# Kernel optimization log

Measured on AMD Instinct MI355X. Metric: run time of the kernel, lower is better.

## Reference

```python
import jax, jax.numpy as jnp
import numpy as np

VOCAB, D = 100000, 300
B, L = 256, 1000
H, C = 512, 5


def setup_inputs() -> dict:
    key = jax.random.key(0)
    ks = jax.random.split(key, 9)
    emb = jax.random.normal(ks[0], (VOCAB, D), dtype=jnp.float32) * 0.1
    W1 = jax.random.normal(ks[1], (D, H), dtype=jnp.float32) * (1.0 / np.sqrt(D))
    b1 = jnp.zeros((H,), dtype=jnp.float32)
    W2 = jax.random.normal(ks[2], (H, H), dtype=jnp.float32) * (1.0 / np.sqrt(H))
    b2 = jnp.zeros((H,), dtype=jnp.float32)
    W3 = jax.random.normal(ks[3], (H, C), dtype=jnp.float32) * (1.0 / np.sqrt(H))
    b3 = jnp.zeros((C,), dtype=jnp.float32)
    docs = jax.random.randint(ks[4], (B, L), 0, VOCAB, dtype=jnp.int32)
    doc_lens = jax.random.randint(ks[5], (B,), 1, L + 1, dtype=jnp.int32)
    return {"embeddings": emb, "W1": W1, "b1": b1, "W2": W2, "b2": b2,
            "W3": W3, "b3": b3, "docs": docs, "doc_lens": doc_lens}


def reference(embeddings, W1, b1, W2, b2, W3, b3, docs, doc_lens):
    # Fused gather + segment-mean: [B, L, D] -> [B, D]
    gathered = embeddings[docs]                       # [B, L, D]
    avg = gathered.sum(axis=1) / doc_lens.astype(jnp.float32)[:, None]  # [B, D]
    # MLP: in -> hidden (ReLU) -> hidden (ReLU) -> classes
    h = jax.nn.relu(avg @ W1 + b1)
    h = jax.nn.relu(h @ W2 + b2)
    return h @ W3 + b3                                # [B, C]
```

## Files before the change

### kernel.cpp

```cpp
#include <hip/hip_runtime.h>

#define VOCAB 100000
#define D     300
#define B     256
#define L     1000
#define H     512
#define C     5

#define D4f    (D / 4)
#define NPH    8
#define RW     1563
#define SELCAP 384

#define WS_PARTIAL 0
#define WS_AVG     (B * 8 * D)
#define WS_H1      (WS_AVG + B * D)
#define WS_H2      (WS_H1 + B * H)

__global__ __launch_bounds__(320) void gather_phased_kernel(
    const float* __restrict__ emb, const int* __restrict__ docs,
    float* __restrict__ partial) {
  const int bid = blockIdx.x;
  const int x = bid & 7;
  const int j = bid >> 3;
  const int t = threadIdx.x;
  const int g = t / 80;
  const int lane = t - g * 80;

  __shared__ int    s_raw[2][L];
  __shared__ int    s_sel[2][SELCAP];
  __shared__ int    s_cnt[2][NPH];
  __shared__ int    s_off[2][NPH + 1];
  __shared__ float4 sred[4][2][D4f];

  for (int i = t; i < 2 * L; i += 320) {
    const int dd = i < L ? 0 : 1;
    const int ii = dd ? i - L : i;
    s_raw[dd][ii] = docs[(size_t)(j * 2 + dd) * L + ii];
  }
  if (t < 2 * NPH) s_cnt[t >> 3][t & 7] = 0;
  __syncthreads();

  for (int i = t; i < 2 * L; i += 320) {
    const int dd = i < L ? 0 : 1;
    const int idx = s_raw[dd][dd ? i - L : i];
    const int r = idx / RW;
    if ((r & 7) == x) atomicAdd(&s_cnt[dd][r >> 3], 1);
  }
  __syncthreads();
  if (t < 2) {
    int acc = 0;
#pragma unroll
    for (int p = 0; p < NPH; ++p) { s_off[t][p] = acc; acc += s_cnt[t][p]; }
    s_off[t][NPH] = acc;
  }
  __syncthreads();
  if (t < 2 * NPH) s_cnt[t >> 3][t & 7] = 0;
  __syncthreads();

  for (int i = t; i < 2 * L; i += 320) {
    const int dd = i < L ? 0 : 1;
    const int idx = s_raw[dd][dd ? i - L : i];
    const int r = idx / RW;
    if ((r & 7) == x) {
      const int pos = s_off[dd][r >> 3] + atomicAdd(&s_cnt[dd][r >> 3], 1);
      s_sel[dd][pos] = idx;
    }
  }
  __syncthreads();

  float4 a0 = make_float4(0.f, 0.f, 0.f, 0.f);
  float4 a1 = make_float4(0.f, 0.f, 0.f, 0.f);
  if (lane < D4f) {
    for (int p = 0; p < NPH; ++p) {
      {
        const int s = s_off[0][p], e = s_off[0][p + 1];
        for (int i = s + g; i < e; i += 4) {
          const float4 v = reinterpret_cast<const float4*>(
              emb + (size_t)s_sel[0][i] * D)[lane];
          a0.x += v.x; a0.y += v.y; a0.z += v.z; a0.w += v.w;
        }
      }
      {
        const int s = s_off[1][p], e = s_off[1][p + 1];
        for (int i = s + g; i < e; i += 4) {
          const float4 v = reinterpret_cast<const float4*>(
              emb + (size_t)s_sel[1][i] * D)[lane];
          a1.x += v.x; a1.y += v.y; a1.z += v.z; a1.w += v.w;
        }
      }
    }
    sred[g][0][lane] = a0;
    sred[g][1][lane] = a1;
  }
  __syncthreads();

  if (t < 2 * D4f) {
    const int dd = t / D4f, c4 = t - dd * D4f;
    float ax = 0.f, ay = 0.f, az = 0.f, aw = 0.f;
#pragma unroll
    for (int gg = 0; gg < 4; ++gg) {
      const float4 v = sred[gg][dd][c4];
      ax += v.x; ay += v.y; az += v.z; aw += v.w;
    }
    reinterpret_cast<float4*>(partial +
                              (size_t)((j * 2 + dd) * 8 + x) * D)[c4] =
        make_float4(ax, ay, az, aw);
  }
}

__global__ __launch_bounds__(128) void avg_kernel(
    const float* __restrict__ partial, const int* __restrict__ dlen,
    float* __restrict__ avg) {
  const int b = blockIdx.x;
  const int t = threadIdx.x;
  if (t < D4f) {
    const float4* p =
        reinterpret_cast<const float4*>(partial) + (size_t)b * 8 * D4f + t;
    float4 v[8];
#pragma unroll
    for (int xx = 0; xx < 8; ++xx) v[xx] = p[xx * D4f];
    float ax = 0.f, ay = 0.f, az = 0.f, aw = 0.f;
#pragma unroll
    for (int xx = 0; xx < 8; ++xx) {
      ax += v[xx].x; ay += v[xx].y; az += v[xx].z; aw += v[xx].w;
    }
    const float inv = 1.f / (float)dlen[b];
    reinterpret_cast<float4*>(avg + (size_t)b * D)[t] =
        make_float4(ax * inv, ay * inv, az * inv, aw * inv);
  }
}

__global__ __launch_bounds__(1024) void l1_kernel(
    const float* __restrict__ avg, const float* __restrict__ W1,
    const float* __restrict__ b1, float* __restrict__ h1) {
  const int dq = blockIdx.x;
  const int cq = blockIdx.y;
  const int t = threadIdx.x;

  __shared__ float4 s_avg[16][D4f];
  __shared__ float  s_w[D][32];
  __shared__ float  s_comb[8][16][32];

  for (int o = t; o < D * 8; o += 1024) {
    const int k = o >> 3, c4 = o & 7;
    *reinterpret_cast<float4*>(&s_w[k][c4 * 4]) =
        *reinterpret_cast<const float4*>(W1 + (size_t)k * H + cq * 32 + c4 * 4);
  }
  for (int o = t; o < 16 * D4f; o += 1024) {
    const int doc = o / D4f, c4 = o - doc * D4f;
    s_avg[doc][c4] =
        reinterpret_cast<const float4*>(avg + (size_t)(dq * 16 + doc) * D)[c4];
  }
  __syncthreads();

  {
    const int doc = t & 15;
    const int cg = (t >> 4) & 7;
    const int ks = t >> 7;
    const int nf4 = (ks < 3) ? 10 : 9;
    const int o4 = (ks < 3) ? 10 * ks : 30 + 9 * (ks - 3);
    float ax = 0.f, ay = 0.f, az = 0.f, aw = 0.f;
    for (int j = 0; j < nf4; ++j) {
      const float4 x4 = s_avg[doc][o4 + j];
      const int k = 4 * (o4 + j);
      const float4 w0 = *reinterpret_cast<const float4*>(&s_w[k + 0][cg * 4]);
      const float4 w1 = *reinterpret_cast<const float4*>(&s_w[k + 1][cg * 4]);
      const float4 w2 = *reinterpret_cast<const float4*>(&s_w[k + 2][cg * 4]);
      const float4 w3 = *reinterpret_cast<const float4*>(&s_w[k + 3][cg * 4]);
      ax += x4.x * w0.x + x4.y * w1.x + x4.z * w2.x + x4.w * w3.x;
      ay += x4.x * w0.y + x4.y * w1.y + x4.z * w2.y + x4.w * w3.y;
      az += x4.x * w0.z + x4.y * w1.z + x4.z * w2.z + x4.w * w3.z;
      aw += x4.x * w0.w + x4.y * w1.w + x4.z * w2.w + x4.w * w3.w;
    }
    *reinterpret_cast<float4*>(&s_comb[ks][doc][cg * 4]) =
        make_float4(ax, ay, az, aw);
  }
  __syncthreads();

  if (t < 512) {
    const int dd = t >> 5, col = t & 31;
    float v = b1[cq * 32 + col];
#pragma unroll
    for (int s = 0; s < 8; ++s) v += s_comb[s][dd][col];
    h1[(size_t)(dq * 16 + dd) * H + cq * 32 + col] = fmaxf(v, 0.f);
  }
}

__global__ __launch_bounds__(1024) void l2_kernel(
    const float* __restrict__ h1, const float* __restrict__ W2,
    const float* __restrict__ b2, float* __restrict__ h2) {
  const int dq = blockIdx.x;
  const int cq = blockIdx.y;
  const int t = threadIdx.x;

  __shared__ float4 s_x[16][H / 4];
  __shared__ float  s_w[H][32];
  __shared__ float  s_comb[8][16][32];

  for (int o = t; o < H * 8; o += 1024) {
    const int k = o >> 3, c4 = o & 7;
    *reinterpret_cast<float4*>(&s_w[k][c4 * 4]) =
        *reinterpret_cast<const float4*>(W2 + (size_t)k * H + cq * 32 + c4 * 4);
  }
  for (int o = t; o < 16 * (H / 4); o += 1024) {
    const int doc = o >> 7, c4 = o & 127;
    s_x[doc][c4] =
        reinterpret_cast<const float4*>(h1 + (size_t)(dq * 16 + doc) * H)[c4];
  }
  __syncthreads();

  {
    const int doc = t & 15;
    const int cg = (t >> 4) & 7;
    const int ks = t >> 7;
    float ax = 0.f, ay = 0.f, az = 0.f, aw = 0.f;
    for (int j = 0; j < 16; ++j) {
      const int kk = ks * 16 + j;
      const float4 x4 = s_x[doc][kk];
      const int k = 4 * kk;
      const float4 w0 = *reinterpret_cast<const float4*>(&s_w[k + 0][cg * 4]);
      const float4 w1 = *reinterpret_cast<const float4*>(&s_w[k + 1][cg * 4]);
      const float4 w2 = *reinterpret_cast<const float4*>(&s_w[k + 2][cg * 4]);
      const float4 w3 = *reinterpret_cast<const float4*>(&s_w[k + 3][cg * 4]);
      ax += x4.x * w0.x + x4.y * w1.x + x4.z * w2.x + x4.w * w3.x;
      ay += x4.x * w0.y + x4.y * w1.y + x4.z * w2.y + x4.w * w3.y;
      az += x4.x * w0.z + x4.y * w1.z + x4.z * w2.z + x4.w * w3.z;
      aw += x4.x * w0.w + x4.y * w1.w + x4.z * w2.w + x4.w * w3.w;
    }
    *reinterpret_cast<float4*>(&s_comb[ks][doc][cg * 4]) =
        make_float4(ax, ay, az, aw);
  }
  __syncthreads();

  if (t < 512) {
    const int dd = t >> 5, col = t & 31;
    float v = b2[cq * 32 + col];
#pragma unroll
    for (int s = 0; s < 8; ++s) v += s_comb[s][dd][col];
    h2[(size_t)(dq * 16 + dd) * H + cq * 32 + col] = fmaxf(v, 0.f);
  }
}

__global__ __launch_bounds__(64) void head_kernel(
    const float* __restrict__ h2, const float* __restrict__ W3,
    const float* __restrict__ b3, float* __restrict__ out) {
  const int b = blockIdx.x;
  const int l = threadIdx.x;
  float acc[C] = {0.f, 0.f, 0.f, 0.f, 0.f};
#pragma unroll
  for (int i = 0; i < H / 64; ++i) {
    const int h = i * 64 + l;
    const float v = h2[(size_t)b * H + h];
#pragma unroll
    for (int c = 0; c < C; ++c) acc[c] += v * W3[h * C + c];
  }
#pragma unroll
  for (int c = 0; c < C; ++c) {
    float a = acc[c];
#pragma unroll
    for (int off = 32; off > 0; off >>= 1) a += __shfl_down(a, off);
    if (l == 0) out[b * C + c] = a + b3[c];
  }
}

extern "C" void kernel_launch(void* const* d_in, const int* in_sizes, int n_in,
                              void* d_out, int out_size, void* d_ws,
                              size_t ws_size, hipStream_t stream) {
  const float* emb  = (const float*)d_in[0];
  const float* W1   = (const float*)d_in[1];
  const float* b1   = (const float*)d_in[2];
  const float* W2   = (const float*)d_in[3];
  const float* b2   = (const float*)d_in[4];
  const float* W3   = (const float*)d_in[5];
  const float* b3   = (const float*)d_in[6];
  const int*   docs = (const int*)d_in[7];
  const int*   dlen = (const int*)d_in[8];
  float* out = (float*)d_out;

  float* ws = (float*)d_ws;
  float* partial = ws + WS_PARTIAL;
  float* avg = ws + WS_AVG;
  float* h1  = ws + WS_H1;
  float* h2  = ws + WS_H2;

  gather_phased_kernel<<<B / 2 * 8, 320, 0, stream>>>(emb, docs, partial);
  avg_kernel<<<B, 128, 0, stream>>>(partial, dlen, avg);
  dim3 gl(16, 16);
  l1_kernel<<<gl, 1024, 0, stream>>>(avg, W1, b1, h1);
  l2_kernel<<<gl, 1024, 0, stream>>>(h1, W2, b2, h2);
  head_kernel<<<B, 64, 0, stream>>>(h2, W3, b3, out);
}
```

Before: 60.68 us.

## Fuse partial reduction via atomics and merge head into second MLP layer

Gather blocks now atomically add their partial sums straight into the average buffer, which removes the separate avg reduction kernel and its partial buffer. The divide by document length moves into the first MLP layer's load. The classifier head is folded into the second layer: each block computes a partial logit from its 32 hidden columns and atomically adds it into the output. A zero kernel is added to clear the accumulators, so launch count goes from five to four, at the cost of float atomics and a non-deterministic summation order.

```diff
diff --git a/kernel.cpp b/kernel.cpp
--- a/kernel.cpp
+++ b/kernel.cpp
@@ -11,15 +11,21 @@
 #define NPH    8
 #define RW     1563
 #define SELCAP 384
-
-#define WS_PARTIAL 0
-#define WS_AVG     (B * 8 * D)
-#define WS_H1      (WS_AVG + B * D)
-#define WS_H2      (WS_H1 + B * H)
+#define NBLK   (B / 2 * 8)
+
+#define WS_AVG 0
+#define WS_H1  (B * D)
+
+__global__ __launch_bounds__(256) void zero_kernel(float* __restrict__ avg,
+                                                   float* __restrict__ out) {
+  const int i = blockIdx.x * 256 + threadIdx.x;
+  if (i < B * D) avg[i] = 0.f;
+  if (i < B * C) out[i] = 0.f;
+}
 
 __global__ __launch_bounds__(320) void gather_phased_kernel(
     const float* __restrict__ emb, const int* __restrict__ docs,
-    float* __restrict__ partial) {
+    float* __restrict__ avg) {
   const int bid = blockIdx.x;
   const int x = bid & 7;
   const int j = bid >> 3;
@@ -103,44 +109,29 @@
       const float4 v = sred[gg][dd][c4];
       ax += v.x; ay += v.y; az += v.z; aw += v.w;
     }
-    reinterpret_cast<float4*>(partial +
-                              (size_t)((j * 2 + dd) * 8 + x) * D)[c4] =
-        make_float4(ax, ay, az, aw);
-  }
-}
-
-__global__ __launch_bounds__(128) void avg_kernel(
-    const float* __restrict__ partial, const int* __restrict__ dlen,
-    float* __restrict__ avg) {
-  const int b = blockIdx.x;
-  const int t = threadIdx.x;
-  if (t < D4f) {
-    const float4* p =
-        reinterpret_cast<const float4*>(partial) + (size_t)b * 8 * D4f + t;
-    float4 v[8];
-#pragma unroll
-    for (int xx = 0; xx < 8; ++xx) v[xx] = p[xx * D4f];
-    float ax = 0.f, ay = 0.f, az = 0.f, aw = 0.f;
-#pragma unroll
-    for (int xx = 0; xx < 8; ++xx) {
-      ax += v[xx].x; ay += v[xx].y; az += v[xx].z; aw += v[xx].w;
-    }
-    const float inv = 1.f / (float)dlen[b];
-    reinterpret_cast<float4*>(avg + (size_t)b * D)[t] =
-        make_float4(ax * inv, ay * inv, az * inv, aw * inv);
+    float* dst = avg + (size_t)(j * 2 + dd) * D + c4 * 4;
+    atomicAdd(dst + 0, ax);
+    atomicAdd(dst + 1, ay);
+    atomicAdd(dst + 2, az);
+    atomicAdd(dst + 3, aw);
   }
 }
 
 __global__ __launch_bounds__(1024) void l1_kernel(
-    const float* __restrict__ avg, const float* __restrict__ W1,
-    const float* __restrict__ b1, float* __restrict__ h1) {
+    const float* __restrict__ avg, const int* __restrict__ dlen,
+    const float* __restrict__ W1, const float* __restrict__ b1,
+    float* __restrict__ h1) {
   const int dq = blockIdx.x;
   const int cq = blockIdx.y;
   const int t = threadIdx.x;
 
+  __shared__ float  s_inv[16];
   __shared__ float4 s_avg[16][D4f];
   __shared__ float  s_w[D][32];
   __shared__ float  s_comb[8][16][32];
+
+  if (t < 16) s_inv[t] = 1.f / (float)dlen[dq * 16 + t];
+  __syncthreads();
 
   for (int o = t; o < D * 8; o += 1024) {
     const int k = o >> 3, c4 = o & 7;
@@ -149,8 +140,10 @@
   }
   for (int o = t; o < 16 * D4f; o += 1024) {
     const int doc = o / D4f, c4 = o - doc * D4f;
-    s_avg[doc][c4] =
+    const float4 v =
         reinterpret_cast<const float4*>(avg + (size_t)(dq * 16 + doc) * D)[c4];
+    const float inv = s_inv[doc];
+    s_avg[doc][c4] = make_float4(v.x * inv, v.y * inv, v.z * inv, v.w * inv);
   }
   __syncthreads();
 
@@ -187,9 +180,10 @@
   }
 }
 
-__global__ __launch_bounds__(1024) void l2_kernel(
+__global__ __launch_bounds__(1024) void l2_head_kernel(
     const float* __restrict__ h1, const float* __restrict__ W2,
-    const float* __restrict__ b2, float* __restrict__ h2) {
+    const float* __restrict__ b2, const float* __restrict__ W3,
+    const float* __restrict__ b3, float* __restrict__ out) {
   const int dq = blockIdx.x;
   const int cq = blockIdx.y;
   const int t = threadIdx.x;
@@ -197,6 +191,7 @@
   __shared__ float4 s_x[16][H / 4];
   __shared__ float  s_w[H][32];
   __shared__ float  s_comb[8][16][32];
+  __shared__ float  s_h2t[16][32];
 
   for (int o = t; o < H * 8; o += 1024) {
     const int k = o >> 3, c4 = o & 7;
@@ -238,29 +233,17 @@
     float v = b2[cq * 32 + col];
 #pragma unroll
     for (int s = 0; s < 8; ++s) v += s_comb[s][dd][col];
-    h2[(size_t)(dq * 16 + dd) * H + cq * 32 + col] = fmaxf(v, 0.f);
-  }
-}
-
-__global__ __launch_bounds__(64) void head_kernel(
-    const float* __restrict__ h2, const float* __restrict__ W3,
-    const float* __restrict__ b3, float* __restrict__ out) {
-  const int b = blockIdx.x;
-  const int l = threadIdx.x;
-  float acc[C] = {0.f, 0.f, 0.f, 0.f, 0.f};
-#pragma unroll
-  for (int i = 0; i < H / 64; ++i) {
-    const int h = i * 64 + l;
-    const float v = h2[(size_t)b * H + h];
-#pragma unroll
-    for (int c = 0; c < C; ++c) acc[c] += v * W3[h * C + c];
-  }
-#pragma unroll
-  for (int c = 0; c < C; ++c) {
-    float a = acc[c];
-#pragma unroll
-    for (int off = 32; off > 0; off >>= 1) a += __shfl_down(a, off);
-    if (l == 0) out[b * C + c] = a + b3[c];
+    s_h2t[dd][col] = fmaxf(v, 0.f);
+  }
+  __syncthreads();
+
+  if (t < 16 * C) {
+    const int doc = t / C;
+    const int c = t - doc * C;
+    float a = (cq == 0) ? b3[c] : 0.f;
+#pragma unroll
+    for (int k = 0; k < 32; ++k) a += s_h2t[doc][k] * W3[(cq * 32 + k) * C + c];
+    atomicAdd(&out[(size_t)(dq * 16 + doc) * C + c], a);
   }
 }
 
@@ -279,15 +262,12 @@
   float* out = (float*)d_out;
 
   float* ws = (float*)d_ws;
-  float* partial = ws + WS_PARTIAL;
   float* avg = ws + WS_AVG;
   float* h1  = ws + WS_H1;
-  float* h2  = ws + WS_H2;
-
-  gather_phased_kernel<<<B / 2 * 8, 320, 0, stream>>>(emb, docs, partial);
-  avg_kernel<<<B, 128, 0, stream>>>(partial, dlen, avg);
+
+  zero_kernel<<<(B * D + 255) / 256, 256, 0, stream>>>(avg, out);
+  gather_phased_kernel<<<NBLK, 320, 0, stream>>>(emb, docs, avg);
   dim3 gl(16, 16);
-  l1_kernel<<<gl, 1024, 0, stream>>>(avg, W1, b1, h1);
-  l2_kernel<<<gl, 1024, 0, stream>>>(h1, W2, b2, h2);
-  head_kernel<<<B, 64, 0, stream>>>(h2, W3, b3, out);
-}
+  l1_kernel<<<gl, 1024, 0, stream>>>(avg, dlen, W1, b1, h1);
+  l2_head_kernel<<<gl, 1024, 0, stream>>>(h1, W2, b2, W3, b3, out);
+}
```

After: 66.18 us. +9.1%, slower.

## Fuse output head into layer-2 kernel and use finer gather phases

Applied to the files above, without the earlier changes.

Removes the separate head kernel and the h2 workspace round trip by computing per-block partial class logits from the layer-2 tile in shared memory and accumulating them into the output with atomics. A zeroing kernel is added before the pipeline to initialize the output. The gather kernel's vocabulary phase count is doubled with half-width row ranges, narrowing each phase's working set for better cache locality at the cost of more phase iterations. Atomic float accumulation makes output summation order nondeterministic.

```diff
diff --git a/kernel.cpp b/kernel.cpp
--- a/kernel.cpp
+++ b/kernel.cpp
@@ -8,14 +8,19 @@
 #define C     5
 
 #define D4f    (D / 4)
-#define NPH    8
-#define RW     1563
+#define NPH    16
+#define RW     782
 #define SELCAP 384
+#define NBLK   (B / 2 * 8)
 
 #define WS_PARTIAL 0
 #define WS_AVG     (B * 8 * D)
 #define WS_H1      (WS_AVG + B * D)
-#define WS_H2      (WS_H1 + B * H)
+
+__global__ __launch_bounds__(256) void zero_out_kernel(float* __restrict__ out) {
+  const int i = blockIdx.x * 256 + threadIdx.x;
+  if (i < B * C) out[i] = 0.f;
+}
 
 __global__ __launch_bounds__(320) void gather_phased_kernel(
     const float* __restrict__ emb, const int* __restrict__ docs,
@@ -38,7 +43,7 @@
     const int ii = dd ? i - L : i;
     s_raw[dd][ii] = docs[(size_t)(j * 2 + dd) * L + ii];
   }
-  if (t < 2 * NPH) s_cnt[t >> 3][t & 7] = 0;
+  if (t < 2 * NPH) s_cnt[t / NPH][t % NPH] = 0;
   __syncthreads();
 
   for (int i = t; i < 2 * L; i += 320) {
@@ -55,7 +60,7 @@
     s_off[t][NPH] = acc;
   }
   __syncthreads();
-  if (t < 2 * NPH) s_cnt[t >> 3][t & 7] = 0;
+  if (t < 2 * NPH) s_cnt[t / NPH][t % NPH] = 0;
   __syncthreads();
 
   for (int i = t; i < 2 * L; i += 320) {
@@ -187,9 +192,10 @@
   }
 }
 
-__global__ __launch_bounds__(1024) void l2_kernel(
+__global__ __launch_bounds__(1024) void l2_head_kernel(
     const float* __restrict__ h1, const float* __restrict__ W2,
-    const float* __restrict__ b2, float* __restrict__ h2) {
+    const float* __restrict__ b2, const float* __restrict__ W3,
+    const float* __restrict__ b3, float* __restrict__ out) {
   const int dq = blockIdx.x;
   const int cq = blockIdx.y;
   const int t = threadIdx.x;
@@ -197,6 +203,7 @@
   __shared__ float4 s_x[16][H / 4];
   __shared__ float  s_w[H][32];
   __shared__ float  s_comb[8][16][32];
+  __shared__ float  s_h2t[16][32];
 
   for (int o = t; o < H * 8; o += 1024) {
     const int k = o >> 3, c4 = o & 7;
@@ -238,29 +245,17 @@
     float v = b2[cq * 32 + col];
 #pragma unroll
     for (int s = 0; s < 8; ++s) v += s_comb[s][dd][col];
-    h2[(size_t)(dq * 16 + dd) * H + cq * 32 + col] = fmaxf(v, 0.f);
-  }
-}
-
-__global__ __launch_bounds__(64) void head_kernel(
-    const float* __restrict__ h2, const float* __restrict__ W3,
-    const float* __restrict__ b3, float* __restrict__ out) {
-  const int b = blockIdx.x;
-  const int l = threadIdx.x;
-  float acc[C] = {0.f, 0.f, 0.f, 0.f, 0.f};
-#pragma unroll
-  for (int i = 0; i < H / 64; ++i) {
-    const int h = i * 64 + l;
-    const float v = h2[(size_t)b * H + h];
-#pragma unroll
-    for (int c = 0; c < C; ++c) acc[c] += v * W3[h * C + c];
-  }
-#pragma unroll
-  for (int c = 0; c < C; ++c) {
-    float a = acc[c];
-#pragma unroll
-    for (int off = 32; off > 0; off >>= 1) a += __shfl_down(a, off);
-    if (l == 0) out[b * C + c] = a + b3[c];
+    s_h2t[dd][col] = fmaxf(v, 0.f);
+  }
+  __syncthreads();
+
+  if (t < 16 * C) {
+    const int doc = t / C;
+    const int c = t - doc * C;
+    float a = (cq == 0) ? b3[c] : 0.f;
+#pragma unroll
+    for (int k = 0; k < 32; ++k) a += s_h2t[doc][k] * W3[(cq * 32 + k) * C + c];
+    atomicAdd(&out[(size_t)(dq * 16 + doc) * C + c], a);
   }
 }
 
@@ -282,12 +277,11 @@
   float* partial = ws + WS_PARTIAL;
   float* avg = ws + WS_AVG;
   float* h1  = ws + WS_H1;
-  float* h2  = ws + WS_H2;
-
-  gather_phased_kernel<<<B / 2 * 8, 320, 0, stream>>>(emb, docs, partial);
+
+  zero_out_kernel<<<(B * C + 255) / 256, 256, 0, stream>>>(out);
+  gather_phased_kernel<<<NBLK, 320, 0, stream>>>(emb, docs, partial);
   avg_kernel<<<B, 128, 0, stream>>>(partial, dlen, avg);
   dim3 gl(16, 16);
   l1_kernel<<<gl, 1024, 0, stream>>>(avg, W1, b1, h1);
-  l2_kernel<<<gl, 1024, 0, stream>>>(h1, W2, b2, h2);
-  head_kernel<<<B, 64, 0, stream>>>(h2, W3, b3, out);
-}
+  l2_head_kernel<<<gl, 1024, 0, stream>>>(h1, W2, b2, W3, b3, out);
+}
```

New measurement: 65.68 us. 1.08x slower.
